# Performance work log

Measured on AMD Instinct MI355X. Metric: run time of the kernel, lower is better.

## Reference

```python
import jax, jax.numpy as jnp
import numpy as np

NLEFT = 8
NRIGHT = 8
D = 768
L = 512
R = 512


def _make_lengths(key, n_attr, total):
    # random positive-ish lengths summing exactly to `total`
    w = jax.random.randint(key, (n_attr,), 1, 64).astype(jnp.float32)
    c = jnp.floor(jnp.cumsum(w) / jnp.sum(w) * total).astype(jnp.int32)
    lens = jnp.diff(jnp.concatenate([jnp.zeros((1,), jnp.int32), c]))
    return lens


def setup_inputs() -> dict:
    key = jax.random.key(0)
    ks = jax.random.split(key, 16)
    std = 0.05
    inp = {
        "left_embeddings": jax.random.normal(ks[0], (L, D), jnp.float32),
        "right_embeddings": jax.random.normal(ks[1], (R, D), jnp.float32),
        "left_attrs_len": _make_lengths(ks[2], NLEFT, L),
        "right_attrs_len": _make_lengths(ks[3], NRIGHT, R),
        # HighwayNet token matching params (input_size=D)
        "hw_tok_Wn": jax.random.normal(ks[4], (D, D), jnp.float32) * std,
        "hw_tok_bn": jnp.zeros((D,), jnp.float32),
        "hw_tok_Wg": jax.random.normal(ks[5], (D, D), jnp.float32) * std,
        "hw_tok_bg": jnp.full((D,), -2.0, jnp.float32),
        "lin_tok_W": jax.random.normal(ks[6], (D, 1), jnp.float32) * std,
        "lin_tok_b": jnp.zeros((1,), jnp.float32),
        "attr_emb_left": jax.random.normal(ks[7], (NLEFT, D), jnp.float32) * std,
        "attr_emb_right": jax.random.normal(ks[8], (NRIGHT, D), jnp.float32) * std,
        # entity matching highway (input_size = (nleft+nright)*D)
        "hw_ent_Wn": jax.random.normal(ks[9], ((NLEFT + NRIGHT) * D, (NLEFT + NRIGHT) * D), jnp.float32) * 0.01,
        "hw_ent_bn": jnp.zeros(((NLEFT + NRIGHT) * D,), jnp.float32),
        "hw_ent_Wg": jax.random.normal(ks[10], ((NLEFT + NRIGHT) * D, (NLEFT + NRIGHT) * D), jnp.float32) * 0.01,
        "hw_ent_bg": jnp.full(((NLEFT + NRIGHT) * D,), -2.0, jnp.float32),
        "lin_ent_W": jax.random.normal(ks[11], ((NLEFT + NRIGHT) * D, 2), jnp.float32) * 0.01,
        "lin_ent_b": jnp.zeros((2,), jnp.float32),
        "empty_attr_res": jax.random.normal(ks[12], (D,), jnp.float32) * std,
    }
    return inp


def _highway(x, Wn, bn, Wg, bg):
    h = jax.nn.relu(x @ Wn + bn)
    g = jax.nn.sigmoid(x @ Wg + bg)
    return g * h + (1.0 - g) * x


def _token_matching(left, right, Wn, bn, Wg, bg, Wl, bl):
    # For each left token i: compare = |left_i - right| -> [R, D]
    # weights = softmax over R of linear(highway(compare)); take row at argmax.
    cmp = jnp.abs(left[:, None, :] - right[None, :, :])  # [L, R, D]
    hw = _highway(cmp, Wn, bn, Wg, bg)                    # [L, R, D]
    scores = (hw @ Wl).squeeze(-1) + bl[0]                # [L, R]
    # softmax over R is monotone; argmax of softmax == argmax of scores
    idx = jnp.argmax(scores, axis=1)                      # [L]
    return jnp.take_along_axis(cmp, idx[:, None, None], axis=1).squeeze(1)  # [L, D]


def _attribute_matching(tokens, field_emb, cmp_res, lens, empty_res, n_attr, n_tok):
    # segment ids per token from lens
    starts = jnp.cumsum(lens) - lens                      # [n_attr]
    seg = jnp.sum(jnp.arange(n_tok)[:, None] >= (starts + lens)[None, :], axis=1)  # [n_tok]
    seg = jnp.clip(seg, 0, n_attr - 1)
    # scores = tokens @ field_emb[seg]
    logits = jnp.einsum('td,td->t', tokens, field_emb[seg])  # [n_tok]
    # ragged softmax per segment
    seg_max = jax.ops.segment_max(logits, seg, num_segments=n_attr)
    ex = jnp.exp(logits - seg_max[seg])
    denom = jax.ops.segment_sum(ex, seg, num_segments=n_attr)
    w = ex / denom[seg]                                    # [n_tok]
    res = jax.ops.segment_sum(w[:, None] * cmp_res, seg, num_segments=n_attr)  # [n_attr, D]
    empty = (lens == 0)
    return jnp.where(empty[:, None], empty_res[None, :], res)


def reference(left_embeddings, right_embeddings, left_attrs_len, right_attrs_len,
              hw_tok_Wn, hw_tok_bn, hw_tok_Wg, hw_tok_bg, lin_tok_W, lin_tok_b,
              attr_emb_left, attr_emb_right,
              hw_ent_Wn, hw_ent_bn, hw_ent_Wg, hw_ent_bg, lin_ent_W, lin_ent_b,
              empty_attr_res):
    lcmp = _token_matching(left_embeddings, right_embeddings,
                           hw_tok_Wn, hw_tok_bn, hw_tok_Wg, hw_tok_bg, lin_tok_W, lin_tok_b)
    rcmp = _token_matching(right_embeddings, left_embeddings,
                           hw_tok_Wn, hw_tok_bn, hw_tok_Wg, hw_tok_bg, lin_tok_W, lin_tok_b)
    lrep = _attribute_matching(left_embeddings, attr_emb_left, lcmp,
                               left_attrs_len, empty_attr_res, NLEFT, L)
    rrep = _attribute_matching(right_embeddings, attr_emb_right, rcmp,
                               right_attrs_len, empty_attr_res, NRIGHT, R)
    concat = jnp.concatenate([lrep, rrep], axis=0).reshape(1, -1)  # [1, (nl+nr)*D]
    hw = _highway(concat, hw_ent_Wn, hw_ent_bn, hw_ent_Wg, hw_ent_bg)
    logits = hw @ lin_ent_W + lin_ent_b
    return jax.nn.softmax(logits, axis=1).flatten()
```

## Files before the change

kernel.cpp:

```cpp
#include <hip/hip_runtime.h>
#include <cmath>

#define NL 8
#define NR 8
#define DIM 768
#define LTOK 512
#define RTOK 512
#define EDIM 12288

typedef unsigned short u16;
typedef __bf16 bf16x8 __attribute__((ext_vector_type(8)));
typedef float  f32x4  __attribute__((ext_vector_type(4)));

#define WARR 589824

__device__ __forceinline__ void splitbf(float c, u16& hi, u16& lo) {
    unsigned u  = __builtin_bit_cast(unsigned, c);
    unsigned hb = (u + 0x7FFFu + ((u >> 16) & 1u)) & 0xFFFF0000u;
    hi = (u16)(hb >> 16);
    float l = c - __builtin_bit_cast(float, hb);
    unsigned ul = __builtin_bit_cast(unsigned, l);
    lo = (u16)((ul + 0x7FFFu + ((ul >> 16) & 1u)) >> 16);
}

__global__ __launch_bounds__(256) void wsplit_kernel(
    const float* __restrict__ Wn, const float* __restrict__ Wg, u16* __restrict__ out)
{
    const int d = blockIdx.x * 256 + threadIdx.x;
    const int k = blockIdx.y;
    const size_t src = (size_t)k * DIM + d;
    const size_t fo  = ((size_t)((k >> 5) * 4 + ((k >> 3) & 3)) * DIM + d) * 8 + (k & 7);
    u16 h, l;
    splitbf(Wn[src], h, l);
    out[fo] = h; out[WARR + fo] = l;
    splitbf(Wg[src], h, l);
    out[2 * WARR + fo] = h; out[3 * WARR + fo] = l;
}

__global__ __launch_bounds__(256, 2) void scores_kernel(
    const float* __restrict__ Lg, const float* __restrict__ Rg,
    const u16* __restrict__ wfrag,
    const float* __restrict__ bn, const float* __restrict__ bg,
    const float* __restrict__ Wl,
    float* __restrict__ scores)
{
    __shared__ float lT[64][66];
    __shared__ float rT[4][66];
    __shared__ u16   wLDS[16384];

    const int t    = threadIdx.x;
    const int lane = t & 63;
    const int wid  = t >> 6;
    const int l15  = lane & 15;
    const int q16  = lane >> 4;
    const int i0   = blockIdx.x * 64;
    const int j    = blockIdx.y * 4 + wid;

    float sacc[4][4];
#pragma unroll
    for (int a = 0; a < 4; ++a)
#pragma unroll
        for (int r = 0; r < 4; ++r) sacc[a][r] = 0.f;

    for (int sweep = 0; sweep < 12; ++sweep) {
        const int dg = sweep * 64;
        f32x4 acc[4][2][4];
#pragma unroll
        for (int a = 0; a < 4; ++a)
#pragma unroll
            for (int m = 0; m < 2; ++m)
#pragma unroll
                for (int n = 0; n < 4; ++n) acc[a][m][n] = (f32x4){0.f, 0.f, 0.f, 0.f};

        for (int k0 = 0; k0 < DIM; k0 += 64) {
            __syncthreads();
            {
                const int k32b = k0 >> 5;
#pragma unroll
                for (int it = 0; it < 8; ++it) {
                    int lidx   = it * 256 + t;
                    int chunk  = lidx >> 6;
                    int within = lidx & 63;
                    int a = chunk >> 3, kcl = (chunk >> 2) & 1, q = chunk & 3;
                    const u16* src = wfrag + (size_t)a * WARR +
                        ((size_t)((k32b + kcl) * 4 + q) * DIM + dg + within) * 8;
                    *(float4*)&wLDS[lidx * 8] = *(const float4*)src;
                }
            }
#pragma unroll
            for (int it = 0; it < 4; ++it) {
                int lidx = it * 256 + t;
                int row = lidx >> 4, c4 = (lidx & 15) * 4;
                float4 v = *(const float4*)(Lg + (size_t)(i0 + row) * DIM + k0 + c4);
                lT[row][c4] = v.x; lT[row][c4 + 1] = v.y;
                lT[row][c4 + 2] = v.z; lT[row][c4 + 3] = v.w;
            }
            {
                int row = t >> 6, c = t & 63;
                rT[row][c] = Rg[(size_t)(blockIdx.y * 4 + row) * DIM + k0 + c];
            }
            __syncthreads();

#pragma unroll
            for (int kc = 0; kc < 2; ++kc) {
                const int koff = kc * 32 + q16 * 8;
                float rv[8];
#pragma unroll
                for (int e = 0; e < 8; e += 2) {
                    float2 p = *(const float2*)&rT[wid][koff + e];
                    rv[e] = p.x; rv[e + 1] = p.y;
                }
                bf16x8 ah[4], al[4];
#pragma unroll
                for (int tile = 0; tile < 4; ++tile) {
                    const float* lrow = &lT[tile * 16 + l15][0];
#pragma unroll
                    for (int e = 0; e < 8; e += 2) {
                        float2 lp = *(const float2*)&lrow[koff + e];
                        u16 h0, o0, h1, o1;
                        splitbf(fabsf(lp.x - rv[e]),     h0, o0);
                        splitbf(fabsf(lp.y - rv[e + 1]), h1, o1);
                        ah[tile][e]     = __builtin_bit_cast(__bf16, h0);
                        ah[tile][e + 1] = __builtin_bit_cast(__bf16, h1);
                        al[tile][e]     = __builtin_bit_cast(__bf16, o0);
                        al[tile][e + 1] = __builtin_bit_cast(__bf16, o1);
                    }
                }
#pragma unroll
                for (int mat = 0; mat < 2; ++mat)
#pragma unroll
                    for (int nt = 0; nt < 4; ++nt) {
                        const int bbase = (mat * 2) * 4096 + kc * 2048 + q16 * 512
                                        + (nt * 16 + l15) * 8;
                        bf16x8 whi = *(const bf16x8*)&wLDS[bbase];
                        bf16x8 wlo = *(const bf16x8*)&wLDS[bbase + 4096];
#pragma unroll
                        for (int tile = 0; tile < 4; ++tile) {
                            acc[tile][mat][nt] = __builtin_amdgcn_mfma_f32_16x16x32_bf16(
                                ah[tile], whi, acc[tile][mat][nt], 0, 0, 0);
                            acc[tile][mat][nt] = __builtin_amdgcn_mfma_f32_16x16x32_bf16(
                                al[tile], whi, acc[tile][mat][nt], 0, 0, 0);
                            acc[tile][mat][nt] = __builtin_amdgcn_mfma_f32_16x16x32_bf16(
                                ah[tile], wlo, acc[tile][mat][nt], 0, 0, 0);
                        }
                    }
            }
        }

#pragma unroll
        for (int nt = 0; nt < 4; ++nt) {
            const int dd = dg + nt * 16 + l15;
            const float bnv = bn[dd], bgv = bg[dd], wlv = Wl[dd];
            const float rvv = Rg[(size_t)j * DIM + dd];
#pragma unroll
            for (int tile = 0; tile < 4; ++tile) {
#pragma unroll
                for (int reg = 0; reg < 4; ++reg) {
                    const int i = i0 + tile * 16 + q16 * 4 + reg;
                    float h  = fmaxf(acc[tile][0][nt][reg] + bnv, 0.f);
                    float g  = 1.f / (1.f + __expf(-(acc[tile][1][nt][reg] + bgv)));
                    float cc = fabsf(Lg[(size_t)i * DIM + dd] - rvv);
                    sacc[tile][reg] = fmaf(wlv, fmaf(g, h - cc, cc), sacc[tile][reg]);
                }
            }
        }
    }

#pragma unroll
    for (int tile = 0; tile < 4; ++tile)
#pragma unroll
        for (int reg = 0; reg < 4; ++reg) {
            float v = sacc[tile][reg];
            v += __shfl_xor(v, 1); v += __shfl_xor(v, 2);
            v += __shfl_xor(v, 4); v += __shfl_xor(v, 8);
            if (l15 == 0)
                scores[(size_t)(i0 + tile * 16 + q16 * 4 + reg) * RTOK + j] = v;
        }
}

__global__ __launch_bounds__(64) void argmax_kernel(
    const float* __restrict__ scores, int* __restrict__ idxL, int* __restrict__ idxR)
{
    const int b = blockIdx.x;
    const int t = threadIdx.x;
    const bool isRow = (b < LTOK);
    const int  n = b & (LTOK - 1);

    float best = -INFINITY;
    int   bidx = 0x7fffffff;
    for (int s = t; s < 512; s += 64) {
        float v = isRow ? scores[n * RTOK + s] : scores[s * RTOK + n];
        if (v > best) { best = v; bidx = s; }
    }
#pragma unroll
    for (int off = 32; off; off >>= 1) {
        float ob = __shfl_down(best, off);
        int   oi = __shfl_down(bidx, off);
        if (ob > best || (ob == best && oi < bidx)) { best = ob; bidx = oi; }
    }
    if (t == 0) (isRow ? idxL : idxR)[n] = bidx;
}

__global__ __launch_bounds__(256) void build_cmp_kernel(
    const float* __restrict__ Lg, const float* __restrict__ Rg,
    const int* __restrict__ idxL, const int* __restrict__ idxR,
    float* __restrict__ lcmp, float* __restrict__ rcmp)
{
    const int b = blockIdx.x;
    const int t = threadIdx.x;
    if (b < LTOK) {
        const float* a = Lg + b * DIM;
        const float* c = Rg + idxL[b] * DIM;
        for (int d = t; d < DIM; d += 256) lcmp[b * DIM + d] = fabsf(a[d] - c[d]);
    } else {
        const int jj = b - LTOK;
        const float* a = Rg + jj * DIM;
        const float* c = Lg + idxR[jj] * DIM;
        for (int d = t; d < DIM; d += 256) rcmp[jj * DIM + d] = fabsf(a[d] - c[d]);
    }
}

__global__ __launch_bounds__(256) void attr_match_kernel(
    const float* __restrict__ Lg, const float* __restrict__ Rg,
    const float* __restrict__ lcmp, const float* __restrict__ rcmp,
    const int* __restrict__ lensL, const int* __restrict__ lensR,
    const float* __restrict__ embL, const float* __restrict__ embR,
    const float* __restrict__ emptyRes,
    float* __restrict__ x)
{
    __shared__ float logits[512];
    __shared__ float red[256];

    const int b    = blockIdx.x;
    const int side = b >> 3;
    const int a    = b & 7;
    const int t    = threadIdx.x;

    const int*   lens = side ? lensR : lensL;
    const float* toks = side ? Rg   : Lg;
    const float* cmp  = side ? rcmp : lcmp;
    const float* femb = (side ? embR : embL) + a * DIM;
    float* outp = x + (side * 8 + a) * DIM;

    int start = 0;
    for (int q = 0; q < a; ++q) start += lens[q];
    const int len = lens[a];

    if (len == 0) {
        for (int d = t; d < DIM; d += 256) outp[d] = emptyRes[d];
        return;
    }

    for (int tok = t; tok < len; tok += 256) {
        const float* tr = toks + (start + tok) * DIM;
        float s = 0.f;
        for (int d = 0; d < DIM; ++d) s = fmaf(tr[d], femb[d], s);
        logits[tok] = s;
    }
    __syncthreads();

    float m = -INFINITY;
    for (int tok = t; tok < len; tok += 256) m = fmaxf(m, logits[tok]);
    red[t] = m; __syncthreads();
    for (int off = 128; off; off >>= 1) {
        if (t < off) red[t] = fmaxf(red[t], red[t + off]);
        __syncthreads();
    }
    m = red[0]; __syncthreads();

    float sum = 0.f;
    for (int tok = t; tok < len; tok += 256) {
        float e = expf(logits[tok] - m);
        logits[tok] = e;
        sum += e;
    }
    red[t] = sum; __syncthreads();
    for (int off = 128; off; off >>= 1) {
        if (t < off) red[t] += red[t + off];
        __syncthreads();
    }
    const float inv = 1.f / red[0];
    __syncthreads();

    for (int d = t; d < DIM; d += 256) {
        float accv = 0.f;
        for (int tok = 0; tok < len; ++tok)
            accv = fmaf(logits[tok] * inv, cmp[(start + tok) * DIM + d], accv);
        outp[d] = accv;
    }
}

__global__ __launch_bounds__(256) void ent_partial_kernel(
    const float* __restrict__ Wn, const float* __restrict__ Wg,
    const float* __restrict__ x, float* __restrict__ partial)
{
    __shared__ float xs[384];
    const int ob   = blockIdx.x;
    const int slab = blockIdx.y;
    const int mat  = blockIdx.z;
    const float* W = mat ? Wg : Wn;
    const int t  = threadIdx.x;
    const int o0 = ob * 1024 + t * 4;
    const int in0 = slab * 384;

    for (int i = t; i < 384; i += 256) xs[i] = x[in0 + i];
    __syncthreads();

    float4 acc = {0.f, 0.f, 0.f, 0.f};
    for (int in = 0; in < 384; ++in) {
        const float  xv = xs[in];
        const float4 w  = *(const float4*)(W + (size_t)(in0 + in) * EDIM + o0);
        acc.x = fmaf(xv, w.x, acc.x);
        acc.y = fmaf(xv, w.y, acc.y);
        acc.z = fmaf(xv, w.z, acc.z);
        acc.w = fmaf(xv, w.w, acc.w);
    }
    *(float4*)(partial + ((size_t)mat * 32 + slab) * EDIM + o0) = acc;
}

__global__ __launch_bounds__(256) void ent_reduce_kernel(
    const float* __restrict__ partial, float* __restrict__ hsum)
{
    const int mat = blockIdx.y;
    const int o   = blockIdx.x * 1024 + threadIdx.x * 4;
    float4 acc = {0.f, 0.f, 0.f, 0.f};
    for (int s = 0; s < 32; ++s) {
        const float4 p = *(const float4*)(partial + ((size_t)mat * 32 + s) * EDIM + o);
        acc.x += p.x; acc.y += p.y; acc.z += p.z; acc.w += p.w;
    }
    *(float4*)(hsum + (size_t)mat * EDIM + o) = acc;
}

__global__ __launch_bounds__(256) void finalize_kernel(
    const float* __restrict__ hsum, const float* __restrict__ x,
    const float* __restrict__ bn, const float* __restrict__ bg,
    const float* __restrict__ Wl2, const float* __restrict__ bl2,
    float* __restrict__ out)
{
    __shared__ float r0[256], r1[256];
    const int t = threadIdx.x;
    float l0 = 0.f, l1 = 0.f;
    for (int d = t; d < EDIM; d += 256) {
        float h  = fmaxf(hsum[d] + bn[d], 0.f);
        float gv = 1.f / (1.f + expf(-(hsum[EDIM + d] + bg[d])));
        float hw = gv * h + (1.f - gv) * x[d];
        l0 = fmaf(hw, Wl2[d * 2 + 0], l0);
        l1 = fmaf(hw, Wl2[d * 2 + 1], l1);
    }
    r0[t] = l0; r1[t] = l1; __syncthreads();
    for (int off = 128; off; off >>= 1) {
        if (t < off) { r0[t] += r0[t + off]; r1[t] += r1[t + off]; }
        __syncthreads();
    }
    if (t == 0) {
        float a = r0[0] + bl2[0];
        float b = r1[0] + bl2[1];
        float m  = fmaxf(a, b);
        float ea = expf(a - m), eb = expf(b - m);
        float inv = 1.f / (ea + eb);
        out[0] = ea * inv;
        out[1] = eb * inv;
    }
}

extern "C" void kernel_launch(void* const* d_in, const int* in_sizes, int n_in,
                              void* d_out, int out_size, void* d_ws, size_t ws_size,
                              hipStream_t stream)
{
    const float* Lg     = (const float*)d_in[0];
    const float* Rg     = (const float*)d_in[1];
    const int*   lensL  = (const int*)  d_in[2];
    const int*   lensR  = (const int*)  d_in[3];
    const float* tWn    = (const float*)d_in[4];
    const float* tbn    = (const float*)d_in[5];
    const float* tWg    = (const float*)d_in[6];
    const float* tbg    = (const float*)d_in[7];
    const float* tWl    = (const float*)d_in[8];
    const float* embL   = (const float*)d_in[10];
    const float* embR   = (const float*)d_in[11];
    const float* eWn    = (const float*)d_in[12];
    const float* ebn    = (const float*)d_in[13];
    const float* eWg    = (const float*)d_in[14];
    const float* ebg    = (const float*)d_in[15];
    const float* eWl    = (const float*)d_in[16];
    const float* ebl    = (const float*)d_in[17];
    const float* emptyR = (const float*)d_in[18];
    float* out = (float*)d_out;

    char* ws = (char*)d_ws;
    u16*   wsplit  = (u16*)ws;
    float* scores  = (float*)(ws + 4718592);
    int*   idxL    = (int*)(ws + 5767168);
    int*   idxR    = idxL + 512;
    float* xcat    = (float*)(ws + 5771264);
    float* hsum    = (float*)(ws + 5820416);
    float* lcmp    = (float*)ws;
    float* rcmp    = lcmp + (size_t)LTOK * DIM;
    float* partial = (float*)ws;

    wsplit_kernel<<<dim3(3, 768), 256, 0, stream>>>(tWn, tWg, wsplit);

    scores_kernel<<<dim3(LTOK / 64, RTOK / 4), 256, 0, stream>>>(
        Lg, Rg, wsplit, tbn, tbg, tWl, scores);

    argmax_kernel<<<dim3(LTOK + RTOK), 64, 0, stream>>>(scores, idxL, idxR);

    build_cmp_kernel<<<dim3(LTOK + RTOK), 256, 0, stream>>>(
        Lg, Rg, idxL, idxR, lcmp, rcmp);

    attr_match_kernel<<<dim3(16), 256, 0, stream>>>(
        Lg, Rg, lcmp, rcmp, lensL, lensR, embL, embR, emptyR, xcat);

    ent_partial_kernel<<<dim3(EDIM / 1024, 32, 2), 256, 0, stream>>>(
        eWn, eWg, xcat, partial);

    ent_reduce_kernel<<<dim3(EDIM / 1024, 2), 256, 0, stream>>>(partial, hsum);

    finalize_kernel<<<dim3(1), 256, 0, stream>>>(
        hsum, xcat, ebn, ebg, eWl, ebl, out);
}
```

Measured before the change: 2.416 ms.

## Double-buffer scores kernel with async LDS loads and 32x32 MFMA tiles

Restructures the pairwise scores kernel into a flattened loop over K steps of 32 with double-buffered LDS. Weight fragments are fetched by direct global-to-LDS loads and the next step's left-token tile is prefetched while MFMAs run on the current buffer. It also switches from 16x16x32 to 32x32x16 bf16 MFMA, keeps the whole right-token rows resident in LDS, and rewrites the weight-split kernel to write 16-byte vectors using native bf16 conversion. This aims to hide load latency and halve the barriers per step, at the cost of more LDS, more accumulator registers, and a new fragment layout that must match exactly.

```diff
diff --git a/kernel.cpp b/kernel.cpp
--- a/kernel.cpp
+++ b/kernel.cpp
@@ -7,34 +7,44 @@
 #define LTOK 512
 #define RTOK 512
 #define EDIM 12288
+#define KST 32
 
 typedef unsigned short u16;
 typedef __bf16 bf16x8 __attribute__((ext_vector_type(8)));
-typedef float  f32x4  __attribute__((ext_vector_type(4)));
+typedef float  f32x16 __attribute__((ext_vector_type(16)));
 
 #define WARR 589824
 
 __device__ __forceinline__ void splitbf(float c, u16& hi, u16& lo) {
-    unsigned u  = __builtin_bit_cast(unsigned, c);
-    unsigned hb = (u + 0x7FFFu + ((u >> 16) & 1u)) & 0xFFFF0000u;
-    hi = (u16)(hb >> 16);
-    float l = c - __builtin_bit_cast(float, hb);
-    unsigned ul = __builtin_bit_cast(unsigned, l);
-    lo = (u16)((ul + 0x7FFFu + ((ul >> 16) & 1u)) >> 16);
+    __bf16 h = (__bf16)c;
+    __bf16 l = (__bf16)(c - (float)h);
+    hi = __builtin_bit_cast(u16, h);
+    lo = __builtin_bit_cast(u16, l);
+}
+
+__device__ __forceinline__ void gll16(const void* gsrc, void* lds) {
+    __builtin_amdgcn_global_load_lds(
+        (const __attribute__((address_space(1))) unsigned int*)gsrc,
+        (__attribute__((address_space(3))) unsigned int*)lds, 16, 0, 0);
 }
 
 __global__ __launch_bounds__(256) void wsplit_kernel(
     const float* __restrict__ Wn, const float* __restrict__ Wg, u16* __restrict__ out)
 {
-    const int d = blockIdx.x * 256 + threadIdx.x;
-    const int k = blockIdx.y;
-    const size_t src = (size_t)k * DIM + d;
-    const size_t fo  = ((size_t)((k >> 5) * 4 + ((k >> 3) & 3)) * DIM + d) * 8 + (k & 7);
-    u16 h, l;
-    splitbf(Wn[src], h, l);
-    out[fo] = h; out[WARR + fo] = l;
-    splitbf(Wg[src], h, l);
-    out[2 * WARR + fo] = h; out[3 * WARR + fo] = l;
+    const int gid = blockIdx.x * 256 + threadIdx.x;
+    const int d  = gid % DIM;
+    const int kg = gid / DIM;
+    u16 hn[8], ln[8], hg[8], lg2[8];
+#pragma unroll
+    for (int e = 0; e < 8; ++e) {
+        splitbf(Wn[(size_t)(kg * 8 + e) * DIM + d], hn[e], ln[e]);
+        splitbf(Wg[(size_t)(kg * 8 + e) * DIM + d], hg[e], lg2[e]);
+    }
+    const size_t fo = ((size_t)kg * DIM + d) * 8;
+    *(uint4*)&out[fo]            = *(uint4*)hn;
+    *(uint4*)&out[WARR + fo]     = *(uint4*)ln;
+    *(uint4*)&out[2 * WARR + fo] = *(uint4*)hg;
+    *(uint4*)&out[3 * WARR + fo] = *(uint4*)lg2;
 }
 
 __global__ __launch_bounds__(256, 2) void scores_kernel(
@@ -44,137 +54,183 @@
     const float* __restrict__ Wl,
     float* __restrict__ scores)
 {
-    __shared__ float lT[64][66];
-    __shared__ float rT[4][66];
-    __shared__ u16   wLDS[16384];
+    __shared__ u16   wLDS[2][8192];
+    __shared__ float lT[2][64][34];
+    __shared__ float rT[4][768];
 
     const int t    = threadIdx.x;
     const int lane = t & 63;
     const int wid  = t >> 6;
-    const int l15  = lane & 15;
-    const int q16  = lane >> 4;
+    const int l31  = lane & 31;
+    const int kh   = lane >> 5;
     const int i0   = blockIdx.x * 64;
-    const int j    = blockIdx.y * 4 + wid;
-
-    float sacc[4][4];
-#pragma unroll
-    for (int a = 0; a < 4; ++a)
-#pragma unroll
-        for (int r = 0; r < 4; ++r) sacc[a][r] = 0.f;
-
-    for (int sweep = 0; sweep < 12; ++sweep) {
-        const int dg = sweep * 64;
-        f32x4 acc[4][2][4];
-#pragma unroll
-        for (int a = 0; a < 4; ++a)
-#pragma unroll
-            for (int m = 0; m < 2; ++m)
-#pragma unroll
-                for (int n = 0; n < 4; ++n) acc[a][m][n] = (f32x4){0.f, 0.f, 0.f, 0.f};
-
-        for (int k0 = 0; k0 < DIM; k0 += 64) {
-            __syncthreads();
-            {
-                const int k32b = k0 >> 5;
-#pragma unroll
-                for (int it = 0; it < 8; ++it) {
-                    int lidx   = it * 256 + t;
-                    int chunk  = lidx >> 6;
-                    int within = lidx & 63;
-                    int a = chunk >> 3, kcl = (chunk >> 2) & 1, q = chunk & 3;
-                    const u16* src = wfrag + (size_t)a * WARR +
-                        ((size_t)((k32b + kcl) * 4 + q) * DIM + dg + within) * 8;
-                    *(float4*)&wLDS[lidx * 8] = *(const float4*)src;
-                }
+    const int j0   = blockIdx.y * 4;
+    const int j    = j0 + wid;
+
+    const int rowS = t >> 2;
+    const int cS   = (t & 3) * 8;
+
+#pragma unroll
+    for (int it = 0; it < 3; ++it) {
+        int idx = it * 256 + t;
+        int row = idx / 192;
+        int c4  = (idx - row * 192) * 4;
+        *(float4*)&rT[row][c4] = *(const float4*)(Rg + (size_t)(j0 + row) * DIM + c4);
+    }
+    {
+#pragma unroll
+        for (int it = 0; it < 4; ++it) {
+            int chunk = it * 4 + wid;
+            int arr = chunk >> 2, kg = chunk & 3;
+            const u16* src = wfrag + (size_t)arr * WARR + ((size_t)kg * DIM + lane) * 8;
+            gll16(src, &wLDS[0][chunk * 512]);
+        }
+        float4 a0 = *(const float4*)(Lg + (size_t)(i0 + rowS) * DIM + cS);
+        float4 a1 = *(const float4*)(Lg + (size_t)(i0 + rowS) * DIM + cS + 4);
+        float* dst = &lT[0][rowS][cS];
+        *(float2*)(dst + 0) = make_float2(a0.x, a0.y);
+        *(float2*)(dst + 2) = make_float2(a0.z, a0.w);
+        *(float2*)(dst + 4) = make_float2(a1.x, a1.y);
+        *(float2*)(dst + 6) = make_float2(a1.z, a1.w);
+    }
+    __syncthreads();
+
+    float sacc[2][16];
+#pragma unroll
+    for (int tile = 0; tile < 2; ++tile)
+#pragma unroll
+        for (int r = 0; r < 16; ++r) sacc[tile][r] = 0.f;
+
+    f32x16 acc[2][2][2];
+#pragma unroll
+    for (int tile = 0; tile < 2; ++tile)
+#pragma unroll
+        for (int mat = 0; mat < 2; ++mat)
+#pragma unroll
+            for (int nd = 0; nd < 2; ++nd)
+                for (int r = 0; r < 16; ++r) acc[tile][mat][nd][r] = 0.f;
+
+    int buf = 0, k0 = 0, dg = 0;
+    for (int s = 0; s < 288; ++s) {
+        int k0n = k0 + KST, dgn = dg;
+        const bool last = (k0n == DIM);
+        if (last) { k0n = 0; dgn = dg + 64; }
+        const bool pref = (s < 287);
+
+        float4 a0, a1;
+        if (pref) {
+            const int kgb = k0n >> 3;
+#pragma unroll
+            for (int it = 0; it < 4; ++it) {
+                int chunk = it * 4 + wid;
+                int arr = chunk >> 2, kg = chunk & 3;
+                const u16* src = wfrag + (size_t)arr * WARR +
+                                 ((size_t)(kgb + kg) * DIM + dgn + lane) * 8;
+                gll16(src, &wLDS[buf ^ 1][chunk * 512]);
             }
-#pragma unroll
-            for (int it = 0; it < 4; ++it) {
-                int lidx = it * 256 + t;
-                int row = lidx >> 4, c4 = (lidx & 15) * 4;
-                float4 v = *(const float4*)(Lg + (size_t)(i0 + row) * DIM + k0 + c4);
-                lT[row][c4] = v.x; lT[row][c4 + 1] = v.y;
-                lT[row][c4 + 2] = v.z; lT[row][c4 + 3] = v.w;
-            }
-            {
-                int row = t >> 6, c = t & 63;
-                rT[row][c] = Rg[(size_t)(blockIdx.y * 4 + row) * DIM + k0 + c];
-            }
-            __syncthreads();
-
-#pragma unroll
-            for (int kc = 0; kc < 2; ++kc) {
-                const int koff = kc * 32 + q16 * 8;
+            a0 = *(const float4*)(Lg + (size_t)(i0 + rowS) * DIM + k0n + cS);
+            a1 = *(const float4*)(Lg + (size_t)(i0 + rowS) * DIM + k0n + cS + 4);
+        }
+
+        {
+            const float* rrow = &rT[wid][k0 + kh * 8];
+            const u16* wb = &wLDS[buf][0];
+#pragma unroll
+            for (int kk = 0; kk < 2; ++kk) {
                 float rv[8];
 #pragma unroll
                 for (int e = 0; e < 8; e += 2) {
-                    float2 p = *(const float2*)&rT[wid][koff + e];
+                    float2 p = *(const float2*)(rrow + kk * 16 + e);
                     rv[e] = p.x; rv[e + 1] = p.y;
                 }
-                bf16x8 ah[4], al[4];
-#pragma unroll
-                for (int tile = 0; tile < 4; ++tile) {
-                    const float* lrow = &lT[tile * 16 + l15][0];
+                bf16x8 ah[2], al[2];
+#pragma unroll
+                for (int tile = 0; tile < 2; ++tile) {
+                    const float* lrow = &lT[buf][tile * 32 + l31][kk * 16 + kh * 8];
 #pragma unroll
                     for (int e = 0; e < 8; e += 2) {
-                        float2 lp = *(const float2*)&lrow[koff + e];
-                        u16 h0, o0, h1, o1;
-                        splitbf(fabsf(lp.x - rv[e]),     h0, o0);
-                        splitbf(fabsf(lp.y - rv[e + 1]), h1, o1);
-                        ah[tile][e]     = __builtin_bit_cast(__bf16, h0);
-                        ah[tile][e + 1] = __builtin_bit_cast(__bf16, h1);
-                        al[tile][e]     = __builtin_bit_cast(__bf16, o0);
-                        al[tile][e + 1] = __builtin_bit_cast(__bf16, o1);
+                        float2 lp = *(const float2*)(lrow + e);
+                        float c0 = fabsf(lp.x - rv[e]);
+                        float c1 = fabsf(lp.y - rv[e + 1]);
+                        __bf16 h0 = (__bf16)c0, h1 = (__bf16)c1;
+                        ah[tile][e]     = h0;
+                        ah[tile][e + 1] = h1;
+                        al[tile][e]     = (__bf16)(c0 - (float)h0);
+                        al[tile][e + 1] = (__bf16)(c1 - (float)h1);
                     }
                 }
 #pragma unroll
                 for (int mat = 0; mat < 2; ++mat)
 #pragma unroll
-                    for (int nt = 0; nt < 4; ++nt) {
-                        const int bbase = (mat * 2) * 4096 + kc * 2048 + q16 * 512
-                                        + (nt * 16 + l15) * 8;
-                        bf16x8 whi = *(const bf16x8*)&wLDS[bbase];
-                        bf16x8 wlo = *(const bf16x8*)&wLDS[bbase + 4096];
-#pragma unroll
-                        for (int tile = 0; tile < 4; ++tile) {
-                            acc[tile][mat][nt] = __builtin_amdgcn_mfma_f32_16x16x32_bf16(
-                                ah[tile], whi, acc[tile][mat][nt], 0, 0, 0);
-                            acc[tile][mat][nt] = __builtin_amdgcn_mfma_f32_16x16x32_bf16(
-                                al[tile], whi, acc[tile][mat][nt], 0, 0, 0);
-                            acc[tile][mat][nt] = __builtin_amdgcn_mfma_f32_16x16x32_bf16(
-                                ah[tile], wlo, acc[tile][mat][nt], 0, 0, 0);
+                    for (int nd = 0; nd < 2; ++nd) {
+                        const int base = (mat * 2) * 2048 + (kk * 2 + kh) * 512
+                                       + (nd * 32 + l31) * 8;
+                        bf16x8 whi = *(const bf16x8*)&wb[base];
+                        bf16x8 wlo = *(const bf16x8*)&wb[base + 2048];
+#pragma unroll
+                        for (int tile = 0; tile < 2; ++tile) {
+                            acc[tile][mat][nd] = __builtin_amdgcn_mfma_f32_32x32x16_bf16(
+                                ah[tile], whi, acc[tile][mat][nd], 0, 0, 0);
+                            acc[tile][mat][nd] = __builtin_amdgcn_mfma_f32_32x32x16_bf16(
+                                al[tile], whi, acc[tile][mat][nd], 0, 0, 0);
+                            acc[tile][mat][nd] = __builtin_amdgcn_mfma_f32_32x32x16_bf16(
+                                ah[tile], wlo, acc[tile][mat][nd], 0, 0, 0);
                         }
                     }
             }
         }
 
-#pragma unroll
-        for (int nt = 0; nt < 4; ++nt) {
-            const int dd = dg + nt * 16 + l15;
-            const float bnv = bn[dd], bgv = bg[dd], wlv = Wl[dd];
-            const float rvv = Rg[(size_t)j * DIM + dd];
-#pragma unroll
-            for (int tile = 0; tile < 4; ++tile) {
-#pragma unroll
-                for (int reg = 0; reg < 4; ++reg) {
-                    const int i = i0 + tile * 16 + q16 * 4 + reg;
-                    float h  = fmaxf(acc[tile][0][nt][reg] + bnv, 0.f);
-                    float g  = 1.f / (1.f + __expf(-(acc[tile][1][nt][reg] + bgv)));
-                    float cc = fabsf(Lg[(size_t)i * DIM + dd] - rvv);
-                    sacc[tile][reg] = fmaf(wlv, fmaf(g, h - cc, cc), sacc[tile][reg]);
-                }
+        if (last) {
+#pragma unroll
+            for (int nd = 0; nd < 2; ++nd) {
+                const int dd = dg + nd * 32 + l31;
+                const float bnv = bn[dd], bgv = bg[dd], wlv = Wl[dd];
+                const float rvv = Rg[(size_t)j * DIM + dd];
+#pragma unroll
+                for (int tile = 0; tile < 2; ++tile)
+#pragma unroll
+                    for (int r = 0; r < 16; ++r) {
+                        const int m = (r & 3) + 8 * (r >> 2) + 4 * kh;
+                        const int i = i0 + tile * 32 + m;
+                        float h  = fmaxf(acc[tile][0][nd][r] + bnv, 0.f);
+                        float g  = 1.f / (1.f + __expf(-(acc[tile][1][nd][r] + bgv)));
+                        float cc = fabsf(Lg[(size_t)i * DIM + dd] - rvv);
+                        sacc[tile][r] = fmaf(wlv, fmaf(g, h - cc, cc), sacc[tile][r]);
+                    }
             }
-        }
-    }
-
-#pragma unroll
-    for (int tile = 0; tile < 4; ++tile)
-#pragma unroll
-        for (int reg = 0; reg < 4; ++reg) {
-            float v = sacc[tile][reg];
-            v += __shfl_xor(v, 1); v += __shfl_xor(v, 2);
-            v += __shfl_xor(v, 4); v += __shfl_xor(v, 8);
-            if (l15 == 0)
-                scores[(size_t)(i0 + tile * 16 + q16 * 4 + reg) * RTOK + j] = v;
+#pragma unroll
+            for (int tile = 0; tile < 2; ++tile)
+#pragma unroll
+                for (int mat = 0; mat < 2; ++mat)
+#pragma unroll
+                    for (int nd = 0; nd < 2; ++nd)
+#pragma unroll
+                        for (int r = 0; r < 16; ++r) acc[tile][mat][nd][r] = 0.f;
+        }
+
+        if (pref) {
+            float* dst = &lT[buf ^ 1][rowS][cS];
+            *(float2*)(dst + 0) = make_float2(a0.x, a0.y);
+            *(float2*)(dst + 2) = make_float2(a0.z, a0.w);
+            *(float2*)(dst + 4) = make_float2(a1.x, a1.y);
+            *(float2*)(dst + 6) = make_float2(a1.z, a1.w);
+        }
+        __syncthreads();
+        buf ^= 1; k0 = k0n; dg = dgn;
+    }
+
+#pragma unroll
+    for (int tile = 0; tile < 2; ++tile)
+#pragma unroll
+        for (int r = 0; r < 16; ++r) {
+            float v = sacc[tile][r];
+            v += __shfl_xor(v, 1);  v += __shfl_xor(v, 2);
+            v += __shfl_xor(v, 4);  v += __shfl_xor(v, 8);
+            v += __shfl_xor(v, 16);
+            if (l31 == 0) {
+                const int m = (r & 3) + 8 * (r >> 2) + 4 * kh;
+                scores[(size_t)(i0 + tile * 32 + m) * RTOK + j] = v;
+            }
         }
 }
 
@@ -398,7 +454,7 @@
     float* rcmp    = lcmp + (size_t)LTOK * DIM;
     float* partial = (float*)ws;
 
-    wsplit_kernel<<<dim3(3, 768), 256, 0, stream>>>(tWn, tWg, wsplit);
+    wsplit_kernel<<<dim3(288), 256, 0, stream>>>(tWn, tWg, wsplit);
 
     scores_kernel<<<dim3(LTOK / 64, RTOK / 4), 256, 0, stream>>>(
         Lg, Rg, wsplit, tbn, tbg, tWl, scores);
```

Result: faster. 2.234 ms (-7.6%).
